# Performance work log

Measured on AMD Instinct MI355X. Metric: run time of the kernel, lower is better.

The kernel has to match this reference:

```python
import jax, jax.numpy as jnp
import numpy as np

DIM = 384
NUM_HEADS = 8


def setup_inputs() -> dict:
    key = jax.random.key(0)
    k1, k2, k3, k4 = jax.random.split(key, 4)
    B, N, D = 8, 16384, DIM
    x = jax.random.normal(k1, (B, N, D), dtype=jnp.float32)
    # nn.Linear(dim, 3*dim, bias=False): weight [3D, D]; store transposed [D, 3D]
    W_qkv = jax.random.normal(k2, (D, 3 * D), dtype=jnp.float32) * (1.0 / np.sqrt(D))
    W_proj = jax.random.normal(k3, (D, D), dtype=jnp.float32) * (1.0 / np.sqrt(D))
    b_proj = jax.random.normal(k4, (D,), dtype=jnp.float32) * 0.01
    return {"x": x, "W_qkv": W_qkv, "W_proj": W_proj, "b_proj": b_proj}


def reference(x, W_qkv, W_proj, b_proj):
    B, N, D = x.shape
    H = NUM_HEADS
    C = D // H
    # qkv: [B, N, 3, H, C] -> split; layout matches '(qkv H C)' packing
    qkv = (x @ W_qkv).reshape(B, N, 3, H, C)
    qkv = jnp.transpose(qkv, (2, 0, 3, 1, 4))  # [3, B, H, N, C]
    q = jax.nn.softmax(qkv[0], axis=-1)        # softmax over channel dim C
    k = jax.nn.softmax(qkv[1], axis=2)         # softmax over token dim N (== B H C N softmax last)
    v = qkv[2]
    # context = k^T @ v : [B, H, C, C] — tiny, avoids NxN scores
    context = jnp.einsum('bhnc,bhnd->bhcd', k, v)
    out = jnp.einsum('bhnc,bhcd->bhnd', q, context)  # [B, H, N, C]
    out = jnp.transpose(out, (0, 2, 1, 3)).reshape(B, N, D)  # 'B H N C -> B N (H C)'
    return out @ W_proj + b_proj
```

## Files before the change

kernel.cpp:

```cpp
#include <hip/hip_runtime.h>
#include <math.h>

#define B_ 8
#define N_ 16384
#define D_ 384
#define TD_ 1152
#define M_ (B_*N_)
#define CTXP_ELEMS (B_*8*32*48*48)
#define ZP_ELEMS   (B_*8*32*48)

typedef __attribute__((ext_vector_type(8))) short short8;
typedef __attribute__((ext_vector_type(4))) float f32x4;
typedef __attribute__((ext_vector_type(4))) unsigned short us4;
typedef __attribute__((ext_vector_type(8))) unsigned short us8;

__device__ __forceinline__ unsigned short f2bf(float f){
    union { float f; unsigned u; } v; v.f = f;
    unsigned r = v.u + 0x7FFFu + ((v.u >> 16) & 1u);
    return (unsigned short)(r >> 16);
}

#define MFMA(a,b,c) __builtin_amdgcn_mfma_f32_16x16x32_bf16((a),(b),(c),0,0,0)

__global__ void kP(const float* __restrict__ Wqkv, const float* __restrict__ Wp,
                   unsigned short* __restrict__ WqkvT, unsigned short* __restrict__ WpT)
{
    __shared__ float t[32][33];
    int bi = blockIdx.x;
    const float* src; unsigned short* dst; int ldS, c0, d0;
    if (bi < 432) { src = Wqkv; dst = WqkvT; ldS = 1152; c0 = (bi % 36) * 32; d0 = (bi / 36) * 32; }
    else { bi -= 432; src = Wp; dst = WpT; ldS = 384; c0 = (bi % 12) * 32; d0 = (bi / 12) * 32; }
    const int cx = threadIdx.x & 31, ry = threadIdx.x >> 5;
#pragma unroll
    for (int k = 0; k < 4; ++k) {
        int r = ry + k * 8;
        t[r][cx] = src[(size_t)(d0 + r) * ldS + c0 + cx];
    }
    __syncthreads();
#pragma unroll
    for (int k = 0; k < 4; ++k) {
        int r = ry + k * 8;
        dst[(size_t)(c0 + r) * 384 + d0 + cx] = f2bf(t[cx][r]);
    }
}

__global__ __launch_bounds__(512, 2) void kA(const float* __restrict__ x,
        const unsigned short* __restrict__ WqkvT,
        float* __restrict__ ctxP, float* __restrict__ ZP)
{
    __shared__ __align__(16) unsigned short xs[64 * 392];
    __shared__ __align__(16) unsigned short kv[8 * 96 * 64];

    const int tid = threadIdx.x;
    const int w   = tid >> 6;
    const int l   = tid & 63;
    const int q   = l >> 4;
    const int c16 = l & 15;
    const int blk = blockIdx.x;
    const int b   = blk >> 5;
    const int s   = blk & 31;
    const int tbase = s * 8;
    unsigned short* kvw = kv + w * (96 * 64);

    f32x4 ctxacc[3][3];
    float zp[3] = {0.f, 0.f, 0.f};
#pragma unroll
    for (int i = 0; i < 3; ++i)
#pragma unroll
        for (int j = 0; j < 3; ++j) ctxacc[i][j] = (f32x4){0.f, 0.f, 0.f, 0.f};

    const int st = tid >> 3, sq = tid & 7;

    f32x4 r[12];
    {
        const float* xg = x + ((size_t)b * 16384 + (size_t)tbase * 64 + st) * 384 + sq * 4;
#pragma unroll
        for (int i = 0; i < 12; ++i)
            r[i] = __builtin_nontemporal_load((const f32x4*)(xg + i * 32));
    }

    for (int g = 0; g < 8; ++g) {
        {
            unsigned short* xw = xs + st * 392 + sq * 4;
#pragma unroll
            for (int i = 0; i < 12; ++i) {
                f32x4 v = r[i];
                us4 o; o.x = f2bf(v.x); o.y = f2bf(v.y); o.z = f2bf(v.z); o.w = f2bf(v.w);
                *(us4*)(xw + i * 32) = o;
            }
        }
        __syncthreads();

        if (g + 1 < 8) {
            const float* xg = x + ((size_t)b * 16384 + (size_t)(tbase + g + 1) * 64 + st) * 384 + sq * 4;
#pragma unroll
            for (int i = 0; i < 12; ++i)
                r[i] = __builtin_nontemporal_load((const f32x4*)(xg + i * 32));
        }

        f32x4 kva[4][6];
#pragma unroll
        for (int mt = 0; mt < 4; ++mt)
#pragma unroll
            for (int j = 0; j < 6; ++j) kva[mt][j] = (f32x4){0.f, 0.f, 0.f, 0.f};

#pragma unroll
        for (int ks = 0; ks < 12; ++ks) {
            short8 a[4];
#pragma unroll
            for (int mt = 0; mt < 4; ++mt)
                a[mt] = *(const short8*)(xs + (mt * 16 + c16) * 392 + ks * 32 + q * 8);
#pragma unroll
            for (int j = 0; j < 6; ++j) {
                const int colrow = (j < 3) ? (384 + w * 48 + j * 16 + c16)
                                           : (768 + w * 48 + (j - 3) * 16 + c16);
                short8 bf = *(const short8*)(WqkvT + (size_t)colrow * 384 + ks * 32 + q * 8);
#pragma unroll
                for (int mt = 0; mt < 4; ++mt)
                    kva[mt][j] = MFMA(a[mt], bf, kva[mt][j]);
            }
        }

#pragma unroll
        for (int mt = 0; mt < 4; ++mt) {
            const int chunk = 2 * mt + (q >> 1);
            const int tin = (q & 1) * 4;
#pragma unroll
            for (int j = 0; j < 6; ++j) {
                f32x4 vv = kva[mt][j];
                us4 o;
                int row;
                if (j < 3) {
                    row = j * 16 + c16;
                    float e0 = __expf(vv.x), e1 = __expf(vv.y), e2 = __expf(vv.z), e3 = __expf(vv.w);
                    zp[j] += (e0 + e1) + (e2 + e3);
                    o.x = f2bf(e0); o.y = f2bf(e1); o.z = f2bf(e2); o.w = f2bf(e3);
                } else {
                    row = 48 + (j - 3) * 16 + c16;
                    o.x = f2bf(vv.x); o.y = f2bf(vv.y); o.z = f2bf(vv.z); o.w = f2bf(vv.w);
                }
                *(us4*)(kvw + row * 64 + ((chunk ^ (row & 7)) << 3) + tin) = o;
            }
        }
        __syncthreads();

#pragma unroll
        for (int kt = 0; kt < 2; ++kt) {
            short8 af[3], bf2[3];
#pragma unroll
            for (int i = 0; i < 3; ++i) {
                const int ra = i * 16 + c16;
                af[i]  = *(const short8*)(kvw + ra * 64 + (((kt * 4 + q) ^ (ra & 7)) << 3));
                const int rb = 48 + i * 16 + c16;
                bf2[i] = *(const short8*)(kvw + rb * 64 + (((kt * 4 + q) ^ (rb & 7)) << 3));
            }
#pragma unroll
            for (int ct = 0; ct < 3; ++ct)
#pragma unroll
                for (int dt = 0; dt < 3; ++dt)
                    ctxacc[ct][dt] = MFMA(af[ct], bf2[dt], ctxacc[ct][dt]);
        }
    }

#pragma unroll
    for (int j = 0; j < 3; ++j) {
        float v = zp[j];
        v += __shfl_xor(v, 16);
        v += __shfl_xor(v, 32);
        if (l < 16)
            __builtin_nontemporal_store(v,
                &ZP[((size_t)(b * 8 + w) * 32 + s) * 48 + j * 16 + c16]);
    }
#pragma unroll
    for (int ct = 0; ct < 3; ++ct)
#pragma unroll
        for (int dt = 0; dt < 3; ++dt) {
            const int d  = dt * 16 + c16;
            const int c0 = ct * 16 + q * 4;
            float* dst = ctxP + ((((size_t)(b * 8 + w) * 32 + s) * 48 + d) * 48 + c0);
            __builtin_nontemporal_store(ctxacc[ct][dt], (f32x4*)dst);
        }
}

__global__ void kB(const float* __restrict__ ctxP, const float* __restrict__ ZP,
                   unsigned short* __restrict__ ctxT)
{
    const int e = blockIdx.x * 256 + threadIdx.x;
    const int bh = e / 3072;
    const int r = e % 3072;
    const int d = r >> 6;
    const int c = r & 63;
    float v = 0.f;
    if (c < 48) {
        float sum = 0.f, zs = 0.f;
#pragma unroll
        for (int s = 0; s < 32; ++s) {
            sum += __builtin_nontemporal_load(
                       ctxP + ((((size_t)bh * 32 + s) * 48 + d) * 48 + c));
            zs  += ZP[((size_t)bh * 32 + s) * 48 + c];
        }
        v = sum / zs;
    }
    ctxT[e] = f2bf(v);
}

__global__ __launch_bounds__(256, 2) void kC(const float* __restrict__ x,
        const unsigned short* __restrict__ WqkvT,
        const unsigned short* __restrict__ ctxT,
        const unsigned short* __restrict__ WpT,
        const float* __restrict__ bp, float* __restrict__ out)
{
    __shared__ __align__(16) unsigned short xs[32 * 392];
    __shared__ __align__(16) unsigned short qs[32 * 520];

    const int tid = threadIdx.x;
    const int w   = tid >> 6;
    const int l   = tid & 63;
    const int q   = l >> 4;
    const int c16 = l & 15;
    const int blk = blockIdx.x;
    const size_t tok0 = (size_t)blk * 32;
    const int b = blk >> 9;

    {
        const int st = tid >> 3, sq = tid & 7;
        const float* xg = x + (tok0 + st) * 384 + sq * 4;
        unsigned short* xw = xs + st * 392 + sq * 4;
#pragma unroll
        for (int i = 0; i < 12; ++i) {
            f32x4 v = __builtin_nontemporal_load((const f32x4*)(xg + i * 32));
            us4 o; o.x = f2bf(v.x); o.y = f2bf(v.y); o.z = f2bf(v.z); o.w = f2bf(v.w);
            *(us4*)(xw + i * 32) = o;
        }
    }
    __syncthreads();

    f32x4 acc[2][6];
#pragma unroll
    for (int mt = 0; mt < 2; ++mt)
#pragma unroll
        for (int j = 0; j < 6; ++j) acc[mt][j] = (f32x4){0.f, 0.f, 0.f, 0.f};

#pragma unroll
    for (int ks = 0; ks < 12; ++ks) {
        short8 a0 = *(const short8*)(xs + (c16) * 392 + ks * 32 + q * 8);
        short8 a1 = *(const short8*)(xs + (16 + c16) * 392 + ks * 32 + q * 8);
#pragma unroll
        for (int j = 0; j < 6; ++j) {
            const int nt = w * 6 + j;
            short8 bf = *(const short8*)(WqkvT + (size_t)(nt * 16 + c16) * 384 + ks * 32 + q * 8);
            acc[0][j] = MFMA(a0, bf, acc[0][j]);
            acc[1][j] = MFMA(a1, bf, acc[1][j]);
        }
    }
    __syncthreads();

#pragma unroll
    for (int hh = 0; hh < 2; ++hh) {
        const int h = 2 * w + hh;
        f32x4 e[2][3];
#pragma unroll
        for (int mt = 0; mt < 2; ++mt)
#pragma unroll
            for (int jj = 0; jj < 3; ++jj) {
                f32x4 vv = acc[mt][hh * 3 + jj];
                e[mt][jj].x = __expf(vv.x); e[mt][jj].y = __expf(vv.y);
                e[mt][jj].z = __expf(vv.z); e[mt][jj].w = __expf(vv.w);
            }
#pragma unroll
        for (int mt = 0; mt < 2; ++mt)
#pragma unroll
            for (int r = 0; r < 4; ++r) {
                float ss = e[mt][0][r] + e[mt][1][r] + e[mt][2][r];
                ss += __shfl_xor(ss, 1); ss += __shfl_xor(ss, 2);
                ss += __shfl_xor(ss, 4); ss += __shfl_xor(ss, 8);
                const float inv = 1.0f / ss;
                e[mt][0][r] *= inv; e[mt][1][r] *= inv; e[mt][2][r] *= inv;
            }
#pragma unroll
        for (int mt = 0; mt < 2; ++mt)
#pragma unroll
            for (int jj = 0; jj < 3; ++jj) {
                const int c = jj * 16 + c16;
#pragma unroll
                for (int r = 0; r < 4; ++r) {
                    const int t = mt * 16 + q * 4 + r;
                    qs[t * 520 + h * 64 + c] = f2bf(e[mt][jj][r]);
                }
            }
    }
    {
        const int t = l & 31, hp = l >> 5;
        const int h = 2 * w + hp;
        us8 z8 = {0, 0, 0, 0, 0, 0, 0, 0};
        *(us8*)(qs + t * 520 + h * 64 + 48) = z8;
    }
    __syncthreads();

#pragma unroll
    for (int hh = 0; hh < 2; ++hh) {
        const int h = 2 * w + hh;
        f32x4 y[2][3];
#pragma unroll
        for (int mt = 0; mt < 2; ++mt)
#pragma unroll
            for (int dt = 0; dt < 3; ++dt) y[mt][dt] = (f32x4){0.f, 0.f, 0.f, 0.f};
#pragma unroll
        for (int ks = 0; ks < 2; ++ks) {
            short8 a0 = *(const short8*)(qs + (c16) * 520 + h * 64 + ks * 32 + q * 8);
            short8 a1 = *(const short8*)(qs + (16 + c16) * 520 + h * 64 + ks * 32 + q * 8);
#pragma unroll
            for (int dt = 0; dt < 3; ++dt) {
                short8 bf = *(const short8*)(ctxT + ((size_t)(b * 8 + h) * 48 + dt * 16 + c16) * 64 + ks * 32 + q * 8);
                y[0][dt] = MFMA(a0, bf, y[0][dt]);
                y[1][dt] = MFMA(a1, bf, y[1][dt]);
            }
        }
#pragma unroll
        for (int mt = 0; mt < 2; ++mt)
#pragma unroll
            for (int dt = 0; dt < 3; ++dt) {
                const int dcol = h * 48 + dt * 16 + c16;
#pragma unroll
                for (int r = 0; r < 4; ++r) {
                    const int t = mt * 16 + q * 4 + r;
                    xs[t * 392 + dcol] = f2bf(y[mt][dt][r]);
                }
            }
    }
    __syncthreads();

    f32x4 po[2][6];
#pragma unroll
    for (int mt = 0; mt < 2; ++mt)
#pragma unroll
        for (int j = 0; j < 6; ++j) po[mt][j] = (f32x4){0.f, 0.f, 0.f, 0.f};

#pragma unroll
    for (int ks = 0; ks < 12; ++ks) {
        short8 a0 = *(const short8*)(xs + (c16) * 392 + ks * 32 + q * 8);
        short8 a1 = *(const short8*)(xs + (16 + c16) * 392 + ks * 32 + q * 8);
#pragma unroll
        for (int j = 0; j < 6; ++j) {
            const int nt = w * 6 + j;
            short8 bf = *(const short8*)(WpT + (size_t)(nt * 16 + c16) * 384 + ks * 32 + q * 8);
            po[0][j] = MFMA(a0, bf, po[0][j]);
            po[1][j] = MFMA(a1, bf, po[1][j]);
        }
    }

#pragma unroll
    for (int j = 0; j < 6; ++j) {
        const int col = (w * 6 + j) * 16 + c16;
        const float bv = bp[col];
#pragma unroll
        for (int mt = 0; mt < 2; ++mt)
#pragma unroll
            for (int r = 0; r < 4; ++r) {
                const int t = mt * 16 + q * 4 + r;
                __builtin_nontemporal_store(po[mt][j][r] + bv,
                                            &out[(tok0 + t) * 384 + col]);
            }
    }
}

extern "C" void kernel_launch(void* const* d_in, const int* in_sizes, int n_in,
                              void* d_out, int out_size, void* d_ws, size_t ws_size,
                              hipStream_t stream)
{
    (void)in_sizes; (void)n_in; (void)out_size; (void)ws_size;
    const float* x    = (const float*)d_in[0];
    const float* Wqkv = (const float*)d_in[1];
    const float* Wp   = (const float*)d_in[2];
    const float* bp   = (const float*)d_in[3];
    float* out = (float*)d_out;

    char* p = (char*)d_ws;
    float* ctxP = (float*)p;                     p += (size_t)CTXP_ELEMS * 4;
    float* ZP   = (float*)p;                     p += (size_t)ZP_ELEMS * 4;
    unsigned short* WqkvT = (unsigned short*)p;  p += (size_t)TD_ * D_ * 2;
    unsigned short* WpT   = (unsigned short*)p;  p += (size_t)D_ * D_ * 2;
    unsigned short* ctxT  = (unsigned short*)p;

    kP<<<dim3(576), dim3(256), 0, stream>>>(Wqkv, Wp, WqkvT, WpT);
    kA<<<dim3(256), dim3(512), 0, stream>>>(x, WqkvT, ctxP, ZP);
    kB<<<dim3(768), dim3(256), 0, stream>>>(ctxP, ZP, ctxT);
    kC<<<dim3(4096), dim3(256), 0, stream>>>(x, WqkvT, ctxT, WpT, bp, out);
}
```

Measured before the change: 845.5 us.

## Fold normalized context into projection weights and split kA into more blocks

Replaces the context-reduction kernel with one that reduces the partial contexts, normalizes them and multiplies by the projection weight. This yields a per-batch combined matrix G = ctx·Wp, so kC applies softmax(q) directly against G and skips the separate q·ctx MFMA stage and its shared buffer. kA now uses 32-token groups across 512 blocks with a smaller LDS footprint and higher occupancy bounds. The cost is a serial 64-block kG with scalar FMA work, plus per-batch G reads in kC instead of one shared Wp.

After: 1.260 ms. 1.49x slower.

```diff
diff --git a/kernel.cpp b/kernel.cpp
--- a/kernel.cpp
+++ b/kernel.cpp
@@ -5,9 +5,9 @@
 #define N_ 16384
 #define D_ 384
 #define TD_ 1152
-#define M_ (B_*N_)
-#define CTXP_ELEMS (B_*8*32*48*48)
-#define ZP_ELEMS   (B_*8*32*48)
+#define S_ 64
+#define CTXP_ELEMS (B_*8*S_*48*48)
+#define ZP_ELEMS   (B_*8*S_*48)
 
 typedef __attribute__((ext_vector_type(8))) short short8;
 typedef __attribute__((ext_vector_type(4))) float f32x4;
@@ -18,6 +18,10 @@
     union { float f; unsigned u; } v; v.f = f;
     unsigned r = v.u + 0x7FFFu + ((v.u >> 16) & 1u);
     return (unsigned short)(r >> 16);
+}
+__device__ __forceinline__ float bf2f(unsigned short h){
+    union { unsigned u; float f; } v; v.u = ((unsigned)h) << 16;
+    return v.f;
 }
 
 #define MFMA(a,b,c) __builtin_amdgcn_mfma_f32_16x16x32_bf16((a),(b),(c),0,0,0)
@@ -44,12 +48,12 @@
     }
 }
 
-__global__ __launch_bounds__(512, 2) void kA(const float* __restrict__ x,
+__global__ __launch_bounds__(512, 4) void kA(const float* __restrict__ x,
         const unsigned short* __restrict__ WqkvT,
         float* __restrict__ ctxP, float* __restrict__ ZP)
 {
-    __shared__ __align__(16) unsigned short xs[64 * 392];
-    __shared__ __align__(16) unsigned short kv[8 * 96 * 64];
+    __shared__ __align__(16) unsigned short xs[32 * 392];
+    __shared__ __align__(16) unsigned short kv[8 * 96 * 32];
 
     const int tid = threadIdx.x;
     const int w   = tid >> 6;
@@ -57,10 +61,9 @@
     const int q   = l >> 4;
     const int c16 = l & 15;
     const int blk = blockIdx.x;
-    const int b   = blk >> 5;
-    const int s   = blk & 31;
-    const int tbase = s * 8;
-    unsigned short* kvw = kv + w * (96 * 64);
+    const int b   = blk >> 6;
+    const int s   = blk & 63;
+    unsigned short* kvw = kv + w * (96 * 32);
 
     f32x4 ctxacc[3][3];
     float zp[3] = {0.f, 0.f, 0.f};
@@ -69,46 +72,46 @@
 #pragma unroll
         for (int j = 0; j < 3; ++j) ctxacc[i][j] = (f32x4){0.f, 0.f, 0.f, 0.f};
 
-    const int st = tid >> 3, sq = tid & 7;
-
-    f32x4 r[12];
+    const int st = tid >> 4, sq = tid & 15;
+
+    f32x4 r[6];
     {
-        const float* xg = x + ((size_t)b * 16384 + (size_t)tbase * 64 + st) * 384 + sq * 4;
-#pragma unroll
-        for (int i = 0; i < 12; ++i)
-            r[i] = __builtin_nontemporal_load((const f32x4*)(xg + i * 32));
+        const float* xg = x + ((size_t)b * 16384 + (size_t)s * 256 + st) * 384 + sq * 4;
+#pragma unroll
+        for (int i = 0; i < 6; ++i)
+            r[i] = __builtin_nontemporal_load((const f32x4*)(xg + i * 64));
     }
 
     for (int g = 0; g < 8; ++g) {
         {
             unsigned short* xw = xs + st * 392 + sq * 4;
 #pragma unroll
-            for (int i = 0; i < 12; ++i) {
+            for (int i = 0; i < 6; ++i) {
                 f32x4 v = r[i];
                 us4 o; o.x = f2bf(v.x); o.y = f2bf(v.y); o.z = f2bf(v.z); o.w = f2bf(v.w);
-                *(us4*)(xw + i * 32) = o;
+                *(us4*)(xw + i * 64) = o;
             }
         }
         __syncthreads();
 
         if (g + 1 < 8) {
-            const float* xg = x + ((size_t)b * 16384 + (size_t)(tbase + g + 1) * 64 + st) * 384 + sq * 4;
-#pragma unroll
-            for (int i = 0; i < 12; ++i)
-                r[i] = __builtin_nontemporal_load((const f32x4*)(xg + i * 32));
-        }
-
-        f32x4 kva[4][6];
-#pragma unroll
-        for (int mt = 0; mt < 4; ++mt)
+            const float* xg = x + ((size_t)b * 16384 + (size_t)s * 256 + (g + 1) * 32 + st) * 384 + sq * 4;
+#pragma unroll
+            for (int i = 0; i < 6; ++i)
+                r[i] = __builtin_nontemporal_load((const f32x4*)(xg + i * 64));
+        }
+
+        f32x4 kva[2][6];
+#pragma unroll
+        for (int mt = 0; mt < 2; ++mt)
 #pragma unroll
             for (int j = 0; j < 6; ++j) kva[mt][j] = (f32x4){0.f, 0.f, 0.f, 0.f};
 
 #pragma unroll
         for (int ks = 0; ks < 12; ++ks) {
-            short8 a[4];
-#pragma unroll
-            for (int mt = 0; mt < 4; ++mt)
+            short8 a[2];
+#pragma unroll
+            for (int mt = 0; mt < 2; ++mt)
                 a[mt] = *(const short8*)(xs + (mt * 16 + c16) * 392 + ks * 32 + q * 8);
 #pragma unroll
             for (int j = 0; j < 6; ++j) {
@@ -116,13 +119,13 @@
                                            : (768 + w * 48 + (j - 3) * 16 + c16);
                 short8 bf = *(const short8*)(WqkvT + (size_t)colrow * 384 + ks * 32 + q * 8);
 #pragma unroll
-                for (int mt = 0; mt < 4; ++mt)
+                for (int mt = 0; mt < 2; ++mt)
                     kva[mt][j] = MFMA(a[mt], bf, kva[mt][j]);
             }
         }
 
 #pragma unroll
-        for (int mt = 0; mt < 4; ++mt) {
+        for (int mt = 0; mt < 2; ++mt) {
             const int chunk = 2 * mt + (q >> 1);
             const int tin = (q & 1) * 4;
 #pragma unroll
@@ -139,20 +142,19 @@
                     row = 48 + (j - 3) * 16 + c16;
                     o.x = f2bf(vv.x); o.y = f2bf(vv.y); o.z = f2bf(vv.z); o.w = f2bf(vv.w);
                 }
-                *(us4*)(kvw + row * 64 + ((chunk ^ (row & 7)) << 3) + tin) = o;
+                *(us4*)(kvw + row * 32 + ((chunk ^ (row & 3)) << 3) + tin) = o;
             }
         }
         __syncthreads();
 
-#pragma unroll
-        for (int kt = 0; kt < 2; ++kt) {
+        {
             short8 af[3], bf2[3];
 #pragma unroll
             for (int i = 0; i < 3; ++i) {
                 const int ra = i * 16 + c16;
-                af[i]  = *(const short8*)(kvw + ra * 64 + (((kt * 4 + q) ^ (ra & 7)) << 3));
+                af[i]  = *(const short8*)(kvw + ra * 32 + ((q ^ (ra & 3)) << 3));
                 const int rb = 48 + i * 16 + c16;
-                bf2[i] = *(const short8*)(kvw + rb * 64 + (((kt * 4 + q) ^ (rb & 7)) << 3));
+                bf2[i] = *(const short8*)(kvw + rb * 32 + ((q ^ (rb & 3)) << 3));
             }
 #pragma unroll
             for (int ct = 0; ct < 3; ++ct)
@@ -169,7 +171,7 @@
         v += __shfl_xor(v, 32);
         if (l < 16)
             __builtin_nontemporal_store(v,
-                &ZP[((size_t)(b * 8 + w) * 32 + s) * 48 + j * 16 + c16]);
+                &ZP[((size_t)(b * 8 + w) * S_ + s) * 48 + j * 16 + c16]);
     }
 #pragma unroll
     for (int ct = 0; ct < 3; ++ct)
@@ -177,41 +179,64 @@
         for (int dt = 0; dt < 3; ++dt) {
             const int d  = dt * 16 + c16;
             const int c0 = ct * 16 + q * 4;
-            float* dst = ctxP + ((((size_t)(b * 8 + w) * 32 + s) * 48 + d) * 48 + c0);
+            float* dst = ctxP + (((size_t)(b * 8 + w) * S_ + s) * 2304 + d * 48 + c0);
             __builtin_nontemporal_store(ctxacc[ct][dt], (f32x4*)dst);
         }
 }
 
-__global__ void kB(const float* __restrict__ ctxP, const float* __restrict__ ZP,
-                   unsigned short* __restrict__ ctxT)
-{
-    const int e = blockIdx.x * 256 + threadIdx.x;
-    const int bh = e / 3072;
-    const int r = e % 3072;
-    const int d = r >> 6;
-    const int c = r & 63;
-    float v = 0.f;
-    if (c < 48) {
-        float sum = 0.f, zs = 0.f;
-#pragma unroll
-        for (int s = 0; s < 32; ++s) {
-            sum += __builtin_nontemporal_load(
-                       ctxP + ((((size_t)bh * 32 + s) * 48 + d) * 48 + c));
-            zs  += ZP[((size_t)bh * 32 + s) * 48 + c];
-        }
-        v = sum / zs;
-    }
-    ctxT[e] = f2bf(v);
-}
-
-__global__ __launch_bounds__(256, 2) void kC(const float* __restrict__ x,
+__global__ __launch_bounds__(384) void kG(const float* __restrict__ ctxP,
+        const float* __restrict__ ZP, const unsigned short* __restrict__ WpT,
+        unsigned short* __restrict__ GT)
+{
+    __shared__ float ctxL[2304];
+    __shared__ float zinv[48];
+    const int bh = blockIdx.x, b = bh >> 3, h = bh & 7;
+    const int t = threadIdx.x;
+
+    if (t < 48) {
+        float z = 0.f;
+        for (int s = 0; s < S_; ++s)
+            z += ZP[((size_t)bh * S_ + s) * 48 + t];
+        zinv[t] = 1.0f / z;
+    }
+#pragma unroll
+    for (int i = 0; i < 6; ++i) {
+        const int f = i * 384 + t;
+        float sum = 0.f;
+        for (int s = 0; s < S_; ++s)
+            sum += __builtin_nontemporal_load(ctxP + (size_t)(bh * S_ + s) * 2304 + f);
+        ctxL[f] = sum;
+    }
+    __syncthreads();
+
+    float wpf[48];
+    const unsigned short* wp = WpT + (size_t)t * 384 + h * 48;
+#pragma unroll
+    for (int d = 0; d < 48; ++d) wpf[d] = bf2f(wp[d]);
+
+    unsigned short* gout = GT + ((size_t)b * 384 + t) * 384 + h * 48;
+#pragma unroll
+    for (int c8 = 0; c8 < 6; ++c8) {
+        us8 o;
+#pragma unroll
+        for (int e = 0; e < 8; ++e) {
+            const int c = c8 * 8 + e;
+            float acc = 0.f;
+#pragma unroll
+            for (int d = 0; d < 48; ++d)
+                acc += ctxL[d * 48 + c] * wpf[d];
+            o[e] = f2bf(acc * zinv[c]);
+        }
+        *(us8*)(gout + c8 * 8) = o;
+    }
+}
+
+__global__ __launch_bounds__(256, 4) void kC(const float* __restrict__ x,
         const unsigned short* __restrict__ WqkvT,
-        const unsigned short* __restrict__ ctxT,
-        const unsigned short* __restrict__ WpT,
+        const unsigned short* __restrict__ GT,
         const float* __restrict__ bp, float* __restrict__ out)
 {
     __shared__ __align__(16) unsigned short xs[32 * 392];
-    __shared__ __align__(16) unsigned short qs[32 * 520];
 
     const int tid = threadIdx.x;
     const int w   = tid >> 6;
@@ -285,46 +310,7 @@
 #pragma unroll
                 for (int r = 0; r < 4; ++r) {
                     const int t = mt * 16 + q * 4 + r;
-                    qs[t * 520 + h * 64 + c] = f2bf(e[mt][jj][r]);
-                }
-            }
-    }
-    {
-        const int t = l & 31, hp = l >> 5;
-        const int h = 2 * w + hp;
-        us8 z8 = {0, 0, 0, 0, 0, 0, 0, 0};
-        *(us8*)(qs + t * 520 + h * 64 + 48) = z8;
-    }
-    __syncthreads();
-
-#pragma unroll
-    for (int hh = 0; hh < 2; ++hh) {
-        const int h = 2 * w + hh;
-        f32x4 y[2][3];
-#pragma unroll
-        for (int mt = 0; mt < 2; ++mt)
-#pragma unroll
-            for (int dt = 0; dt < 3; ++dt) y[mt][dt] = (f32x4){0.f, 0.f, 0.f, 0.f};
-#pragma unroll
-        for (int ks = 0; ks < 2; ++ks) {
-            short8 a0 = *(const short8*)(qs + (c16) * 520 + h * 64 + ks * 32 + q * 8);
-            short8 a1 = *(const short8*)(qs + (16 + c16) * 520 + h * 64 + ks * 32 + q * 8);
-#pragma unroll
-            for (int dt = 0; dt < 3; ++dt) {
-                short8 bf = *(const short8*)(ctxT + ((size_t)(b * 8 + h) * 48 + dt * 16 + c16) * 64 + ks * 32 + q * 8);
-                y[0][dt] = MFMA(a0, bf, y[0][dt]);
-                y[1][dt] = MFMA(a1, bf, y[1][dt]);
-            }
-        }
-#pragma unroll
-        for (int mt = 0; mt < 2; ++mt)
-#pragma unroll
-            for (int dt = 0; dt < 3; ++dt) {
-                const int dcol = h * 48 + dt * 16 + c16;
-#pragma unroll
-                for (int r = 0; r < 4; ++r) {
-                    const int t = mt * 16 + q * 4 + r;
-                    xs[t * 392 + dcol] = f2bf(y[mt][dt][r]);
+                    xs[t * 392 + h * 48 + c] = f2bf(e[mt][jj][r]);
                 }
             }
     }
@@ -343,7 +329,7 @@
 #pragma unroll
         for (int j = 0; j < 6; ++j) {
             const int nt = w * 6 + j;
-            short8 bf = *(const short8*)(WpT + (size_t)(nt * 16 + c16) * 384 + ks * 32 + q * 8);
+            short8 bf = *(const short8*)(GT + ((size_t)(b * 384 + nt * 16 + c16)) * 384 + ks * 32 + q * 8);
             po[0][j] = MFMA(a0, bf, po[0][j]);
             po[1][j] = MFMA(a1, bf, po[1][j]);
         }
@@ -380,10 +366,10 @@
     float* ZP   = (float*)p;                     p += (size_t)ZP_ELEMS * 4;
     unsigned short* WqkvT = (unsigned short*)p;  p += (size_t)TD_ * D_ * 2;
     unsigned short* WpT   = (unsigned short*)p;  p += (size_t)D_ * D_ * 2;
-    unsigned short* ctxT  = (unsigned short*)p;
+    unsigned short* GT    = (unsigned short*)p;
 
     kP<<<dim3(576), dim3(256), 0, stream>>>(Wqkv, Wp, WqkvT, WpT);
-    kA<<<dim3(256), dim3(512), 0, stream>>>(x, WqkvT, ctxP, ZP);
-    kB<<<dim3(768), dim3(256), 0, stream>>>(ctxP, ZP, ctxT);
-    kC<<<dim3(4096), dim3(256), 0, stream>>>(x, WqkvT, ctxT, WpT, bp, out);
-}
+    kA<<<dim3(512), dim3(512), 0, stream>>>(x, WqkvT, ctxP, ZP);
+    kG<<<dim3(64), dim3(384), 0, stream>>>(ctxP, ZP, WpT, GT);
+    kC<<<dim3(4096), dim3(256), 0, stream>>>(x, WqkvT, GT, bp, out);
+}
```
